# Performance work log

Measured on AMD Instinct MI355X. Metric: run time of the kernel, lower is better.

## Reference

```python
import jax, jax.numpy as jnp
import numpy as np
from jax import lax

# Geometry constants (stand-in for beijing* globals)
A = 96           # beijingAngleNum
P = 4            # beijingPlanes
DET0, DET1 = 256, 8   # beijingSubDetectorSize [u, v]
NZ, NY, NX = 32, 256, 256  # beijingVolumeSize (nz = P * DET1)
T = 256          # ray integration steps
LAMB = 0.01


def _bilinear(vol, ix, iy):
    # vol: [nz, ny, nx]; ix, iy: [...] index-space coords. Zero outside.
    nz, ny, nx = vol.shape
    x0 = jnp.floor(ix); y0 = jnp.floor(iy)
    fx = (ix - x0).astype(vol.dtype); fy = (iy - y0).astype(vol.dtype)
    x0i = x0.astype(jnp.int32); y0i = y0.astype(jnp.int32)

    def g(yi, xi):
        valid = ((xi >= 0) & (xi < nx) & (yi >= 0) & (yi < ny)).astype(vol.dtype)
        v = vol[:, jnp.clip(yi, 0, ny - 1), jnp.clip(xi, 0, nx - 1)]  # [nz, ...]
        return v * valid

    return (g(y0i, x0i) * (1 - fy) * (1 - fx)
            + g(y0i, x0i + 1) * (1 - fy) * fx
            + g(y0i + 1, x0i) * fy * (1 - fx)
            + g(y0i + 1, x0i + 1) * fy * fx)


def forward_project(vol):
    # vol: [NZ, NY, NX] -> sinogram [A, NZ, DET0], parallel-beam over 180 deg
    angles = jnp.arange(A, dtype=jnp.float32) * (np.pi / A)
    u = jnp.arange(DET0, dtype=jnp.float32) - (DET0 - 1) / 2.0  # detector coord
    t = jnp.arange(T, dtype=jnp.float32) - (T - 1) / 2.0        # along-ray coord

    def per_angle(_, th):
        c, s = jnp.cos(th), jnp.sin(th)
        x = -u[:, None] * s + t[None, :] * c   # [DET0, T]
        y = u[:, None] * c + t[None, :] * s
        samp = _bilinear(vol, x + (NX - 1) / 2.0, y + (NY - 1) / 2.0)  # [NZ,DET0,T]
        return None, samp.sum(-1)  # line integral, [NZ, DET0]

    _, S = lax.scan(per_angle, None, angles)
    return S  # [A, NZ, DET0]


def back_project(S):
    # S: [A, NZ, DET0] -> volume [NZ, NY, NX] (adjoint-style backprojection)
    angles = jnp.arange(A, dtype=jnp.float32) * (np.pi / A)
    yy = jnp.arange(NY, dtype=jnp.float32) - (NY - 1) / 2.0
    xx = jnp.arange(NX, dtype=jnp.float32) - (NX - 1) / 2.0
    Y, X = jnp.meshgrid(yy, xx, indexing='ij')  # [NY, NX]

    def per_angle(acc, inp):
        th, Sa = inp  # Sa: [NZ, DET0]
        c, s = jnp.cos(th), jnp.sin(th)
        ub = -X * s + Y * c + (DET0 - 1) / 2.0  # detector bin coord [NY,NX]
        u0 = jnp.floor(ub)
        fu = (ub - u0).astype(Sa.dtype)
        u0i = u0.astype(jnp.int32)

        def g(ui):
            valid = ((ui >= 0) & (ui < DET0)).astype(Sa.dtype)
            return Sa[:, jnp.clip(ui, 0, DET0 - 1)] * valid  # [NZ,NY,NX]

        val = g(u0i) * (1 - fu) + g(u0i + 1) * fu
        return acc + val, None

    vol0 = jnp.zeros((NZ, NY, NX), dtype=S.dtype)
    vol, _ = lax.scan(per_angle, vol0, (angles, S))
    return vol


def setup_inputs() -> dict:
    key = jax.random.key(0)
    k1, k2 = jax.random.split(key)
    x = jax.random.normal(k1, (1, 1, NZ, NY, NX), dtype=jnp.float32)
    p = jax.random.normal(k2, (1, 1, A * P, DET1, DET0), dtype=jnp.float32)
    return {"x": x, "p": p}


def reference(x, p):
    vol = x[0, 0]                              # [NZ, NY, NX]
    S = forward_project(vol)                   # [A, NZ, DET0] native
    # ForwardProjection wrapper: (A,P,V,U) -> permute -> flat external layout
    ext = S.reshape(A, P, DET1, DET0).transpose(0, 2, 1, 3).reshape(1, 1, A * P, DET1, DET0)
    residual = ext - p
    # BackProjection wrapper: undo external layout back to native
    res_native = residual.reshape(A, DET1, P, DET0).transpose(0, 2, 1, 3).reshape(A, NZ, DET0)
    volb = back_project(res_native)            # [NZ, NY, NX]
    return (-LAMB * volb)[None, None]          # [1,1,NZ,NY,NX]
```

## Files before the change

### kernel.cpp

```cpp
#include <hip/hip_runtime.h>
#include <hip/hip_fp16.h>

#define A     96
#define DET0  256
#define NZ    32
#define NY    256
#define NX    256
#define T     256
#define LAMB  0.01f

#define TRIG_OFF  0
#define REST_OFF  256
#define VOLB_OFF  786688
#define PART_OFF  1835264
#define RES_ELEMS 786432

__device__ __forceinline__ void accp_mix(float& a0, float& a1, unsigned v, float w) {
    asm("v_fma_mix_f32 %0, %2, %3, %0 op_sel:[0,0,0] op_sel_hi:[1,0,0]\n\t"
        "v_fma_mix_f32 %1, %2, %3, %1 op_sel:[1,0,0] op_sel_hi:[1,0,0]"
        : "+v"(a0), "+v"(a1)
        : "v"(v), "v"(w));
}
__device__ __forceinline__ void acc8h(float* acc, uint4 q, float w) {
    accp_mix(acc[0], acc[1], q.x, w);
    accp_mix(acc[2], acc[3], q.y, w);
    accp_mix(acc[4], acc[5], q.z, w);
    accp_mix(acc[6], acc[7], q.w, w);
}

__global__ __launch_bounds__(256) void k_transpose(const float* __restrict__ src,
                                                   unsigned short* __restrict__ vol_h,
                                                   float* __restrict__ trig,
                                                   const float* __restrict__ p,
                                                   float* __restrict__ res_t) {
    __shared__ float lds[64 * 33];
    const int y   = blockIdx.y;
    const int x0  = blockIdx.x * 64;
    const int tid = threadIdx.x;

    if (blockIdx.x == 0 && y == 0 && tid < A) {
        float th = (float)tid * (float)(3.14159265358979323846 / (double)A);
        trig[2 * tid]     = cosf(th);
        trig[2 * tid + 1] = sinf(th);
    }

    const int xr = tid & 63;
    const int zr = tid >> 6;
    #pragma unroll
    for (int pz = 0; pz < 8; ++pz) {
        int z = pz * 4 + zr;
        lds[xr * 33 + z] = src[(z * NY + y) * NX + x0 + xr];
    }
    __syncthreads();
    const int zw = tid & 31;
    const int xw = tid >> 5;
    #pragma unroll
    for (int px = 0; px < 8; ++px) {
        int xi = px * 8 + xw;
        vol_h[(y * NX + x0 + xi) * NZ + zw] =
            __half_as_ushort(__float2half(lds[xi * 33 + zw]));
    }

    if (y < A) {
        const int a  = y;
        const int u0 = blockIdx.x * 64;
        __syncthreads();
        const int col = tid & 63;
        const int r0  = tid >> 6;
        #pragma unroll
        for (int i = 0; i < 8; ++i) {
            int r = i * 4 + r0;
            lds[r * 65 + col] = p[a * 8192 + r * 256 + u0 + col];
        }
        __syncthreads();
        const int ul = tid >> 2;
        const int zb = (tid & 3) * 8;
        float o[8];
        #pragma unroll
        for (int k = 0; k < 8; ++k) {
            int z = zb + k;
            int r = ((z & 7) << 2) + (z >> 3);
            o[k] = -lds[r * 65 + ul];
        }
        float4* d = (float4*)(res_t + (a * DET0 + u0 + ul) * NZ + zb);
        d[0] = make_float4(o[0], o[1], o[2], o[3]);
        d[1] = make_float4(o[4], o[5], o[6], o[7]);
    }
}

__device__ __forceinline__ void rng(float g, float b, float L, float H,
                                    float& lo, float& hi) {
    if (fabsf(g) > 1e-5f) {
        float r0 = (L - b) / g, r1 = (H - b) / g;
        lo = fminf(r0, r1); hi = fmaxf(r0, r1);
    } else {
        bool in = (b >= L && b <= H);
        lo = in ? -1e9f : 1e9f;
        hi = in ? 1e9f : -1e9f;
    }
}
__device__ __forceinline__ int clampi(float v) {
    return (int)fminf(fmaxf(v, -2.f), 258.f);
}

__device__ __forceinline__ void sample_edge(const char* base, float ix, float iy,
                                            float* acc) {
    float xf = floorf(ix), yf = floorf(iy);
    float fx = ix - xf, fy = iy - yf;
    int x0 = (int)xf, y0 = (int)yf;
    float wx0 = 1.f - fx, wx1 = fx, wy0 = 1.f - fy, wy1 = fy;
    if ((unsigned)x0 >= NX)       wx0 = 0.f;
    if ((unsigned)(x0 + 1) >= NX) wx1 = 0.f;
    if ((unsigned)y0 >= NY)       wy0 = 0.f;
    if ((unsigned)(y0 + 1) >= NY) wy1 = 0.f;
    if ((wx0 == 0.f && wx1 == 0.f) || (wy0 == 0.f && wy1 == 0.f)) return;
    int cx0 = min(max(x0, 0), NX - 1);
    int cx1 = min(max(x0 + 1, 0), NX - 1);
    int cy0 = min(max(y0, 0), NY - 1);
    int cy1 = min(max(y0 + 1, 0), NY - 1);
    uint4 q00 = *(const uint4*)(base + ((size_t)((cy0 << 8) + cx0) << 6));
    uint4 q01 = *(const uint4*)(base + ((size_t)((cy0 << 8) + cx1) << 6));
    uint4 q10 = *(const uint4*)(base + ((size_t)((cy1 << 8) + cx0) << 6));
    uint4 q11 = *(const uint4*)(base + ((size_t)((cy1 << 8) + cx1) << 6));
    acc8h(acc, q00, wy0 * wx0);
    acc8h(acc, q01, wy0 * wx1);
    acc8h(acc, q10, wy1 * wx0);
    acc8h(acc, q11, wy1 * wx1);
}

__global__ __launch_bounds__(256) void k_forward(const unsigned short* __restrict__ vol_h,
                                                 const float* __restrict__ trig,
                                                 float* __restrict__ part) {
    const int tid = threadIdx.x;
    const int a   = blockIdx.z;
    const int u   = blockIdx.x * 64 + (tid >> 2);
    const int zq  = tid & 3;
    const int cid = blockIdx.y;
    const int C   = gridDim.y;

    const float c = trig[2 * a];
    const float s = trig[2 * a + 1];
    const float uu = (float)u - 127.5f;
    const float bx = fmaf(-uu, s, 127.5f);
    const float by = fmaf(uu, c, 127.5f);

    float lo1, hi1, lo2, hi2;
    rng(c, bx, -1.f, 256.f, lo1, hi1);
    rng(s, by, -1.f, 256.f, lo2, hi2);
    float fl = fmaxf(lo1, lo2), fh = fminf(hi1, hi2);
    int F0 = max(0,     clampi(ceilf(fl + 127.5f)));
    int F1 = min(T - 1, clampi(floorf(fh + 127.5f)));
    int len = F1 - F0 + 1; if (len < 0) len = 0;
    int b0 = F0 + (len * cid) / C;
    int b1 = F0 + (len * (cid + 1)) / C - 1;
    rng(c, bx, 1.f, 253.5f, lo1, hi1);
    rng(s, by, 1.f, 253.5f, lo2, hi2);
    float il = fmaxf(lo1, lo2), ih = fminf(hi1, hi2);
    int tI0 = max(clampi(ceilf(il + 127.5f)) + 1, b0);
    int tI1 = min(clampi(floorf(ih + 127.5f)) - 1, b1);
    if (tI0 > tI1) { tI0 = b1 + 1; tI1 = b1; }

    const char* base = (const char*)vol_h + zq * 16;
    float acc[8];
    #pragma unroll
    for (int k = 0; k < 8; ++k) acc[k] = 0.f;

    for (int t = b0; t < tI0; ++t) {
        float ttf = (float)t - 127.5f;
        sample_edge(base, fmaf(ttf, c, bx), fmaf(ttf, s, by), acc);
    }
    for (int t = tI0; t <= tI1; ++t) {
        float ttf = (float)t - 127.5f;
        float ix = fmaf(ttf, c, bx);
        float iy = fmaf(ttf, s, by);
        float xf = floorf(ix), yf = floorf(iy);
        float fx = ix - xf, fy = iy - yf;
        int row = ((int)yf << 8) + (int)xf;
        const char* p0 = base + ((size_t)row << 6);
        uint4 q00 = *(const uint4*)(p0);
        uint4 q01 = *(const uint4*)(p0 + 64);
        uint4 q10 = *(const uint4*)(p0 + 16384);
        uint4 q11 = *(const uint4*)(p0 + 16384 + 64);
        float wx0 = 1.f - fx, wy0 = 1.f - fy;
        acc8h(acc, q00, wy0 * wx0);
        acc8h(acc, q01, wy0 * fx);
        acc8h(acc, q10, fy * wx0);
        acc8h(acc, q11, fy * fx);
    }
    for (int t = tI1 + 1; t <= b1; ++t) {
        float ttf = (float)t - 127.5f;
        sample_edge(base, fmaf(ttf, c, bx), fmaf(ttf, s, by), acc);
    }

    float4* dst = (float4*)(part + (size_t)cid * RES_ELEMS +
                            ((a * DET0 + u) * NZ + zq * 8));
    dst[0] = make_float4(acc[0], acc[1], acc[2], acc[3]);
    dst[1] = make_float4(acc[4], acc[5], acc[6], acc[7]);
}

__global__ __launch_bounds__(256) void k_combine(const float* __restrict__ part,
                                                 float* __restrict__ res_t,
                                                 int C) {
    const int j4 = blockIdx.x * 256 + threadIdx.x;
    float4 v = ((const float4*)res_t)[j4];
    for (int c = 0; c < C; ++c) {
        float4 w = ((const float4*)(part + (size_t)c * RES_ELEMS))[j4];
        v.x += w.x; v.y += w.y; v.z += w.z; v.w += w.w;
    }
    ((float4*)res_t)[j4] = v;
}

__global__ __launch_bounds__(256, 8) void k_backward(const float* __restrict__ res_t,
                                                     const float* __restrict__ trig,
                                                     float* __restrict__ out) {
    __shared__ float ob[32 * 33];
    const int tid = threadIdx.x;
    const int y  = blockIdx.y;
    const int xb = blockIdx.x * 32;
    const int xs = tid >> 3;
    const int zq = tid & 7;
    const char* rbase = (const char*)res_t + zq * 16;
    const float xx = (float)(xb + xs) - 127.5f;
    const float yy = (float)y - 127.5f;

    float4 acc = make_float4(0.f, 0.f, 0.f, 0.f);
    #pragma unroll 4
    for (int a = 0; a < A; ++a) {
        float cc = trig[2 * a];
        float ss = trig[2 * a + 1];
        float ub = fmaf(-xx, ss, fmaf(yy, cc, 127.5f));
        float uf = floorf(ub);
        float fu = ub - uf;
        int i0 = (int)uf;
        float w0 = ((unsigned)i0 < DET0) ? (1.f - fu) : 0.f;
        float w1 = ((unsigned)(i0 + 1) < DET0) ? fu : 0.f;
        int c1 = min(max(i0 + 1, 0), DET0);
        int off = ((a * DET0 + c1) * NZ - NZ) << 2;
        float4 v0 = *(const float4*)(rbase + off);
        float4 v1 = *(const float4*)(rbase + off + 128);
        acc.x = fmaf(w0, v0.x, fmaf(w1, v1.x, acc.x));
        acc.y = fmaf(w0, v0.y, fmaf(w1, v1.y, acc.y));
        acc.z = fmaf(w0, v0.z, fmaf(w1, v1.z, acc.z));
        acc.w = fmaf(w0, v0.w, fmaf(w1, v1.w, acc.w));
    }

    ob[(zq * 4 + 0) * 33 + xs] = acc.x;
    ob[(zq * 4 + 1) * 33 + xs] = acc.y;
    ob[(zq * 4 + 2) * 33 + xs] = acc.z;
    ob[(zq * 4 + 3) * 33 + xs] = acc.w;
    __syncthreads();

    const int z  = tid >> 3;
    const int x4 = (tid & 7) * 4;
    float4 o = make_float4(ob[z * 33 + x4],     ob[z * 33 + x4 + 1],
                           ob[z * 33 + x4 + 2], ob[z * 33 + x4 + 3]);
    float4* dst = (float4*)(out + (size_t)z * (NY * NX) + y * NX + xb + x4);
    *dst = make_float4(-LAMB * o.x, -LAMB * o.y, -LAMB * o.z, -LAMB * o.w);
}

extern "C" void kernel_launch(void* const* d_in, const int* in_sizes, int n_in,
                              void* d_out, int out_size, void* d_ws, size_t ws_size,
                              hipStream_t stream) {
    const float* x = (const float*)d_in[0];
    const float* p = (const float*)d_in[1];
    float* out = (float*)d_out;
    float* ws  = (float*)d_ws;

    float*          trig  = ws + TRIG_OFF;
    float*          res_t = ws + REST_OFF;
    unsigned short* vol_h = (unsigned short*)(ws + VOLB_OFF);
    float*          part  = ws + PART_OFF;

    size_t avail = ws_size / 4;
    int C = 8;
    while (C > 1 && (size_t)PART_OFF + (size_t)C * RES_ELEMS > avail) C >>= 1;

    k_transpose<<<dim3(NX / 64, NY), 256, 0, stream>>>(x, vol_h, trig, p, res_t);
    k_forward  <<<dim3(4, C, A), 256, 0, stream>>>(vol_h, trig, part);
    k_combine  <<<dim3(RES_ELEMS / 4 / 256), 256, 0, stream>>>(part, res_t, C);
    k_backward <<<dim3(NX / 32, NY), 256, 0, stream>>>(res_t, trig, out);
}
```

Before: 192.4 us.

## Fuse four kernels into one persistent cooperative kernel with grid syncs

Replaces the four separate launches (transpose, forward, combine, backward) with a single cooperative kernel of 1024 blocks that walks the same phases, separated by grid.sync(). Each block handles several work units per phase in a persistent-style loop. The aim is to remove the launch overhead and the gaps between kernels. In exchange it pays for grid-wide barriers, is limited to 1024 co-resident blocks (launch bounds 256,4), and fixes C=8 partial buffers without checking the workspace size.

```diff
diff --git a/kernel.cpp b/kernel.cpp
--- a/kernel.cpp
+++ b/kernel.cpp
@@ -1,5 +1,8 @@
 #include <hip/hip_runtime.h>
 #include <hip/hip_fp16.h>
+#include <hip/hip_cooperative_groups.h>
+
+namespace cg = cooperative_groups;
 
 #define A     96
 #define DET0  256
@@ -7,6 +10,7 @@
 #define NY    256
 #define NX    256
 #define T     256
+#define NC    8
 #define LAMB  0.01f
 
 #define TRIG_OFF  0
@@ -26,66 +30,6 @@
     accp_mix(acc[2], acc[3], q.y, w);
     accp_mix(acc[4], acc[5], q.z, w);
     accp_mix(acc[6], acc[7], q.w, w);
-}
-
-__global__ __launch_bounds__(256) void k_transpose(const float* __restrict__ src,
-                                                   unsigned short* __restrict__ vol_h,
-                                                   float* __restrict__ trig,
-                                                   const float* __restrict__ p,
-                                                   float* __restrict__ res_t) {
-    __shared__ float lds[64 * 33];
-    const int y   = blockIdx.y;
-    const int x0  = blockIdx.x * 64;
-    const int tid = threadIdx.x;
-
-    if (blockIdx.x == 0 && y == 0 && tid < A) {
-        float th = (float)tid * (float)(3.14159265358979323846 / (double)A);
-        trig[2 * tid]     = cosf(th);
-        trig[2 * tid + 1] = sinf(th);
-    }
-
-    const int xr = tid & 63;
-    const int zr = tid >> 6;
-    #pragma unroll
-    for (int pz = 0; pz < 8; ++pz) {
-        int z = pz * 4 + zr;
-        lds[xr * 33 + z] = src[(z * NY + y) * NX + x0 + xr];
-    }
-    __syncthreads();
-    const int zw = tid & 31;
-    const int xw = tid >> 5;
-    #pragma unroll
-    for (int px = 0; px < 8; ++px) {
-        int xi = px * 8 + xw;
-        vol_h[(y * NX + x0 + xi) * NZ + zw] =
-            __half_as_ushort(__float2half(lds[xi * 33 + zw]));
-    }
-
-    if (y < A) {
-        const int a  = y;
-        const int u0 = blockIdx.x * 64;
-        __syncthreads();
-        const int col = tid & 63;
-        const int r0  = tid >> 6;
-        #pragma unroll
-        for (int i = 0; i < 8; ++i) {
-            int r = i * 4 + r0;
-            lds[r * 65 + col] = p[a * 8192 + r * 256 + u0 + col];
-        }
-        __syncthreads();
-        const int ul = tid >> 2;
-        const int zb = (tid & 3) * 8;
-        float o[8];
-        #pragma unroll
-        for (int k = 0; k < 8; ++k) {
-            int z = zb + k;
-            int r = ((z & 7) << 2) + (z >> 3);
-            o[k] = -lds[r * 65 + ul];
-        }
-        float4* d = (float4*)(res_t + (a * DET0 + u0 + ul) * NZ + zb);
-        d[0] = make_float4(o[0], o[1], o[2], o[3]);
-        d[1] = make_float4(o[4], o[5], o[6], o[7]);
-    }
 }
 
 __device__ __forceinline__ void rng(float g, float b, float L, float H,
@@ -128,134 +72,206 @@
     acc8h(acc, q11, wy1 * wx1);
 }
 
-__global__ __launch_bounds__(256) void k_forward(const unsigned short* __restrict__ vol_h,
-                                                 const float* __restrict__ trig,
-                                                 float* __restrict__ part) {
+__global__ __launch_bounds__(256, 4) void k_fused(const float* __restrict__ src,
+                                                  const float* __restrict__ p,
+                                                  float* __restrict__ out,
+                                                  float* __restrict__ ws) {
+    __shared__ float smem[64 * 33];
+    cg::grid_group grid = cg::this_grid();
+    const int bid = blockIdx.x;
     const int tid = threadIdx.x;
-    const int a   = blockIdx.z;
-    const int u   = blockIdx.x * 64 + (tid >> 2);
-    const int zq  = tid & 3;
-    const int cid = blockIdx.y;
-    const int C   = gridDim.y;
-
-    const float c = trig[2 * a];
-    const float s = trig[2 * a + 1];
-    const float uu = (float)u - 127.5f;
-    const float bx = fmaf(-uu, s, 127.5f);
-    const float by = fmaf(uu, c, 127.5f);
-
-    float lo1, hi1, lo2, hi2;
-    rng(c, bx, -1.f, 256.f, lo1, hi1);
-    rng(s, by, -1.f, 256.f, lo2, hi2);
-    float fl = fmaxf(lo1, lo2), fh = fminf(hi1, hi2);
-    int F0 = max(0,     clampi(ceilf(fl + 127.5f)));
-    int F1 = min(T - 1, clampi(floorf(fh + 127.5f)));
-    int len = F1 - F0 + 1; if (len < 0) len = 0;
-    int b0 = F0 + (len * cid) / C;
-    int b1 = F0 + (len * (cid + 1)) / C - 1;
-    rng(c, bx, 1.f, 253.5f, lo1, hi1);
-    rng(s, by, 1.f, 253.5f, lo2, hi2);
-    float il = fmaxf(lo1, lo2), ih = fminf(hi1, hi2);
-    int tI0 = max(clampi(ceilf(il + 127.5f)) + 1, b0);
-    int tI1 = min(clampi(floorf(ih + 127.5f)) - 1, b1);
-    if (tI0 > tI1) { tI0 = b1 + 1; tI1 = b1; }
-
-    const char* base = (const char*)vol_h + zq * 16;
-    float acc[8];
-    #pragma unroll
-    for (int k = 0; k < 8; ++k) acc[k] = 0.f;
-
-    for (int t = b0; t < tI0; ++t) {
-        float ttf = (float)t - 127.5f;
-        sample_edge(base, fmaf(ttf, c, bx), fmaf(ttf, s, by), acc);
-    }
-    for (int t = tI0; t <= tI1; ++t) {
-        float ttf = (float)t - 127.5f;
-        float ix = fmaf(ttf, c, bx);
-        float iy = fmaf(ttf, s, by);
-        float xf = floorf(ix), yf = floorf(iy);
-        float fx = ix - xf, fy = iy - yf;
-        int row = ((int)yf << 8) + (int)xf;
-        const char* p0 = base + ((size_t)row << 6);
-        uint4 q00 = *(const uint4*)(p0);
-        uint4 q01 = *(const uint4*)(p0 + 64);
-        uint4 q10 = *(const uint4*)(p0 + 16384);
-        uint4 q11 = *(const uint4*)(p0 + 16384 + 64);
-        float wx0 = 1.f - fx, wy0 = 1.f - fy;
-        acc8h(acc, q00, wy0 * wx0);
-        acc8h(acc, q01, wy0 * fx);
-        acc8h(acc, q10, fy * wx0);
-        acc8h(acc, q11, fy * fx);
-    }
-    for (int t = tI1 + 1; t <= b1; ++t) {
-        float ttf = (float)t - 127.5f;
-        sample_edge(base, fmaf(ttf, c, bx), fmaf(ttf, s, by), acc);
-    }
-
-    float4* dst = (float4*)(part + (size_t)cid * RES_ELEMS +
-                            ((a * DET0 + u) * NZ + zq * 8));
-    dst[0] = make_float4(acc[0], acc[1], acc[2], acc[3]);
-    dst[1] = make_float4(acc[4], acc[5], acc[6], acc[7]);
-}
-
-__global__ __launch_bounds__(256) void k_combine(const float* __restrict__ part,
-                                                 float* __restrict__ res_t,
-                                                 int C) {
-    const int j4 = blockIdx.x * 256 + threadIdx.x;
-    float4 v = ((const float4*)res_t)[j4];
-    for (int c = 0; c < C; ++c) {
-        float4 w = ((const float4*)(part + (size_t)c * RES_ELEMS))[j4];
-        v.x += w.x; v.y += w.y; v.z += w.z; v.w += w.w;
-    }
-    ((float4*)res_t)[j4] = v;
-}
-
-__global__ __launch_bounds__(256, 8) void k_backward(const float* __restrict__ res_t,
-                                                     const float* __restrict__ trig,
-                                                     float* __restrict__ out) {
-    __shared__ float ob[32 * 33];
-    const int tid = threadIdx.x;
-    const int y  = blockIdx.y;
-    const int xb = blockIdx.x * 32;
-    const int xs = tid >> 3;
-    const int zq = tid & 7;
-    const char* rbase = (const char*)res_t + zq * 16;
-    const float xx = (float)(xb + xs) - 127.5f;
-    const float yy = (float)y - 127.5f;
-
-    float4 acc = make_float4(0.f, 0.f, 0.f, 0.f);
-    #pragma unroll 4
-    for (int a = 0; a < A; ++a) {
-        float cc = trig[2 * a];
-        float ss = trig[2 * a + 1];
-        float ub = fmaf(-xx, ss, fmaf(yy, cc, 127.5f));
-        float uf = floorf(ub);
-        float fu = ub - uf;
-        int i0 = (int)uf;
-        float w0 = ((unsigned)i0 < DET0) ? (1.f - fu) : 0.f;
-        float w1 = ((unsigned)(i0 + 1) < DET0) ? fu : 0.f;
-        int c1 = min(max(i0 + 1, 0), DET0);
-        int off = ((a * DET0 + c1) * NZ - NZ) << 2;
-        float4 v0 = *(const float4*)(rbase + off);
-        float4 v1 = *(const float4*)(rbase + off + 128);
-        acc.x = fmaf(w0, v0.x, fmaf(w1, v1.x, acc.x));
-        acc.y = fmaf(w0, v0.y, fmaf(w1, v1.y, acc.y));
-        acc.z = fmaf(w0, v0.z, fmaf(w1, v1.z, acc.z));
-        acc.w = fmaf(w0, v0.w, fmaf(w1, v1.w, acc.w));
-    }
-
-    ob[(zq * 4 + 0) * 33 + xs] = acc.x;
-    ob[(zq * 4 + 1) * 33 + xs] = acc.y;
-    ob[(zq * 4 + 2) * 33 + xs] = acc.z;
-    ob[(zq * 4 + 3) * 33 + xs] = acc.w;
-    __syncthreads();
-
-    const int z  = tid >> 3;
-    const int x4 = (tid & 7) * 4;
-    float4 o = make_float4(ob[z * 33 + x4],     ob[z * 33 + x4 + 1],
-                           ob[z * 33 + x4 + 2], ob[z * 33 + x4 + 3]);
-    float4* dst = (float4*)(out + (size_t)z * (NY * NX) + y * NX + xb + x4);
-    *dst = make_float4(-LAMB * o.x, -LAMB * o.y, -LAMB * o.z, -LAMB * o.w);
+    float*          trig  = ws + TRIG_OFF;
+    float*          res_t = ws + REST_OFF;
+    unsigned short* vol_h = (unsigned short*)(ws + VOLB_OFF);
+    float*          part  = ws + PART_OFF;
+
+    {
+        const int y  = bid >> 2;
+        const int x0 = (bid & 3) * 64;
+
+        if (bid == 0) {
+            if (tid < A) {
+                float th = (float)tid * (float)(3.14159265358979323846 / (double)A);
+                trig[2 * tid]     = cosf(th);
+                trig[2 * tid + 1] = sinf(th);
+            } else if (tid >= 2 * A) {
+                trig[tid] = 0.f;
+            }
+        }
+
+        const int xr = tid & 63;
+        const int zr = tid >> 6;
+        #pragma unroll
+        for (int pz = 0; pz < 8; ++pz) {
+            int z = pz * 4 + zr;
+            smem[xr * 33 + z] = src[(z * NY + y) * NX + x0 + xr];
+        }
+        __syncthreads();
+        const int zw = tid & 31;
+        const int xw = tid >> 5;
+        #pragma unroll
+        for (int px = 0; px < 8; ++px) {
+            int xi = px * 8 + xw;
+            vol_h[(y * NX + x0 + xi) * NZ + zw] =
+                __half_as_ushort(__float2half(smem[xi * 33 + zw]));
+        }
+
+        if (y < A) {
+            const int a  = y;
+            const int u0 = (bid & 3) * 64;
+            __syncthreads();
+            const int col = tid & 63;
+            const int r0  = tid >> 6;
+            #pragma unroll
+            for (int i = 0; i < 8; ++i) {
+                int r = i * 4 + r0;
+                smem[r * 65 + col] = p[a * 8192 + r * 256 + u0 + col];
+            }
+            __syncthreads();
+            const int ul = tid >> 2;
+            const int zb = (tid & 3) * 8;
+            float o[8];
+            #pragma unroll
+            for (int k = 0; k < 8; ++k) {
+                int z = zb + k;
+                int r = ((z & 7) << 2) + (z >> 3);
+                o[k] = -smem[r * 65 + ul];
+            }
+            float4* d = (float4*)(res_t + (a * DET0 + u0 + ul) * NZ + zb);
+            d[0] = make_float4(o[0], o[1], o[2], o[3]);
+            d[1] = make_float4(o[4], o[5], o[6], o[7]);
+        }
+    }
+    grid.sync();
+
+    #pragma unroll 1
+    for (int u3 = 0; u3 < 3; ++u3) {
+        const int unit = bid + u3 * 1024;
+        const int a   = unit >> 5;
+        const int cid = (unit >> 2) & 7;
+        const int ux  = unit & 3;
+        const int u   = ux * 64 + (tid >> 2);
+        const int zq  = tid & 3;
+
+        const float c = trig[2 * a];
+        const float s = trig[2 * a + 1];
+        const float uu = (float)u - 127.5f;
+        const float bx = fmaf(-uu, s, 127.5f);
+        const float by = fmaf(uu, c, 127.5f);
+
+        float lo1, hi1, lo2, hi2;
+        rng(c, bx, -1.f, 256.f, lo1, hi1);
+        rng(s, by, -1.f, 256.f, lo2, hi2);
+        float fl = fmaxf(lo1, lo2), fh = fminf(hi1, hi2);
+        int F0 = max(0,     clampi(ceilf(fl + 127.5f)));
+        int F1 = min(T - 1, clampi(floorf(fh + 127.5f)));
+        int len = F1 - F0 + 1; if (len < 0) len = 0;
+        int b0 = F0 + (len * cid) / NC;
+        int b1 = F0 + (len * (cid + 1)) / NC - 1;
+        rng(c, bx, 1.f, 253.5f, lo1, hi1);
+        rng(s, by, 1.f, 253.5f, lo2, hi2);
+        float il = fmaxf(lo1, lo2), ih = fminf(hi1, hi2);
+        int tI0 = max(clampi(ceilf(il + 127.5f)) + 1, b0);
+        int tI1 = min(clampi(floorf(ih + 127.5f)) - 1, b1);
+        if (tI0 > tI1) { tI0 = b1 + 1; tI1 = b1; }
+
+        const char* base = (const char*)vol_h + zq * 16;
+        float acc[8];
+        #pragma unroll
+        for (int k = 0; k < 8; ++k) acc[k] = 0.f;
+
+        for (int t = b0; t < tI0; ++t) {
+            float ttf = (float)t - 127.5f;
+            sample_edge(base, fmaf(ttf, c, bx), fmaf(ttf, s, by), acc);
+        }
+        for (int t = tI0; t <= tI1; ++t) {
+            float ttf = (float)t - 127.5f;
+            float ix = fmaf(ttf, c, bx);
+            float iy = fmaf(ttf, s, by);
+            float xf = floorf(ix), yf = floorf(iy);
+            float fx = ix - xf, fy = iy - yf;
+            int row = ((int)yf << 8) + (int)xf;
+            const char* p0 = base + ((size_t)row << 6);
+            uint4 q00 = *(const uint4*)(p0);
+            uint4 q01 = *(const uint4*)(p0 + 64);
+            uint4 q10 = *(const uint4*)(p0 + 16384);
+            uint4 q11 = *(const uint4*)(p0 + 16384 + 64);
+            float wx0 = 1.f - fx, wy0 = 1.f - fy;
+            acc8h(acc, q00, wy0 * wx0);
+            acc8h(acc, q01, wy0 * fx);
+            acc8h(acc, q10, fy * wx0);
+            acc8h(acc, q11, fy * fx);
+        }
+        for (int t = tI1 + 1; t <= b1; ++t) {
+            float ttf = (float)t - 127.5f;
+            sample_edge(base, fmaf(ttf, c, bx), fmaf(ttf, s, by), acc);
+        }
+
+        float4* dst = (float4*)(part + (size_t)cid * RES_ELEMS +
+                                ((a * DET0 + u) * NZ + zq * 8));
+        dst[0] = make_float4(acc[0], acc[1], acc[2], acc[3]);
+        dst[1] = make_float4(acc[4], acc[5], acc[6], acc[7]);
+    }
+    grid.sync();
+
+    if (bid < 768) {
+        const int j4 = bid * 256 + tid;
+        float4 v = ((const float4*)res_t)[j4];
+        #pragma unroll
+        for (int c = 0; c < NC; ++c) {
+            float4 w = ((const float4*)(part + (size_t)c * RES_ELEMS))[j4];
+            v.x += w.x; v.y += w.y; v.z += w.z; v.w += w.w;
+        }
+        ((float4*)res_t)[j4] = v;
+    }
+    grid.sync();
+
+    #pragma unroll 1
+    for (int u2 = 0; u2 < 2; ++u2) {
+        const int unit = bid + u2 * 1024;
+        const int y  = unit >> 3;
+        const int xb = (unit & 7) * 32;
+        const int xs = tid >> 3;
+        const int zq = tid & 7;
+        const char* rbase = (const char*)res_t + zq * 16;
+        const float xx = (float)(xb + xs) - 127.5f;
+        const float yy = (float)y - 127.5f;
+
+        float4 acc = make_float4(0.f, 0.f, 0.f, 0.f);
+        #pragma unroll 4
+        for (int a = 0; a < A; ++a) {
+            float cc = trig[2 * a];
+            float ss = trig[2 * a + 1];
+            float ub = fmaf(-xx, ss, fmaf(yy, cc, 127.5f));
+            float uf = floorf(ub);
+            float fu = ub - uf;
+            int i0 = (int)uf;
+            float w0 = ((unsigned)i0 < DET0) ? (1.f - fu) : 0.f;
+            float w1 = ((unsigned)(i0 + 1) < DET0) ? fu : 0.f;
+            int c1 = min(max(i0 + 1, 0), DET0);
+            int off = ((a * DET0 + c1) * NZ - NZ) << 2;
+            float4 v0 = *(const float4*)(rbase + off);
+            float4 v1 = *(const float4*)(rbase + off + 128);
+            acc.x = fmaf(w0, v0.x, fmaf(w1, v1.x, acc.x));
+            acc.y = fmaf(w0, v0.y, fmaf(w1, v1.y, acc.y));
+            acc.z = fmaf(w0, v0.z, fmaf(w1, v1.z, acc.z));
+            acc.w = fmaf(w0, v0.w, fmaf(w1, v1.w, acc.w));
+        }
+
+        __syncthreads();
+        smem[(zq * 4 + 0) * 33 + xs] = acc.x;
+        smem[(zq * 4 + 1) * 33 + xs] = acc.y;
+        smem[(zq * 4 + 2) * 33 + xs] = acc.z;
+        smem[(zq * 4 + 3) * 33 + xs] = acc.w;
+        __syncthreads();
+
+        const int z  = tid >> 3;
+        const int x4 = (tid & 7) * 4;
+        float4 o = make_float4(smem[z * 33 + x4],     smem[z * 33 + x4 + 1],
+                               smem[z * 33 + x4 + 2], smem[z * 33 + x4 + 3]);
+        float4* dst = (float4*)(out + (size_t)z * (NY * NX) + y * NX + xb + x4);
+        *dst = make_float4(-LAMB * o.x, -LAMB * o.y, -LAMB * o.z, -LAMB * o.w);
+    }
 }
 
 extern "C" void kernel_launch(void* const* d_in, const int* in_sizes, int n_in,
@@ -266,17 +282,7 @@
     float* out = (float*)d_out;
     float* ws  = (float*)d_ws;
 
-    float*          trig  = ws + TRIG_OFF;
-    float*          res_t = ws + REST_OFF;
-    unsigned short* vol_h = (unsigned short*)(ws + VOLB_OFF);
-    float*          part  = ws + PART_OFF;
-
-    size_t avail = ws_size / 4;
-    int C = 8;
-    while (C > 1 && (size_t)PART_OFF + (size_t)C * RES_ELEMS > avail) C >>= 1;
-
-    k_transpose<<<dim3(NX / 64, NY), 256, 0, stream>>>(x, vol_h, trig, p, res_t);
-    k_forward  <<<dim3(4, C, A), 256, 0, stream>>>(vol_h, trig, part);
-    k_combine  <<<dim3(RES_ELEMS / 4 / 256), 256, 0, stream>>>(part, res_t, C);
-    k_backward <<<dim3(NX / 32, NY), 256, 0, stream>>>(res_t, trig, out);
-}
+    void* args[] = { (void*)&x, (void*)&p, (void*)&out, (void*)&ws };
+    hipLaunchCooperativeKernel((const void*)k_fused, dim3(1024), dim3(256),
+                               args, 0, stream);
+}
```

New measurement: 578.6 us. 201% more time.
